# Kernel optimization log

Hardware: AMD Instinct MI355X
Metric: run time of the kernel (lower is better)

Reference implementation:

```python
import jax, jax.numpy as jnp
import numpy as np

BETA = 0.5
LAMBDA = 0.5
EPS = 1e-24


def setup_inputs() -> dict:
    key = jax.random.key(0)
    k1, k2 = jax.random.split(key)
    seq = jax.random.normal(k1, (32, 512, 128), dtype=jnp.float32)
    fism_items = jax.random.normal(k2, (32, 2048, 128), dtype=jnp.float32)
    return {"seq": seq, "fism_items": fism_items}


def reference(seq, fism_items):
    # scores: [B, L, N]
    w = jnp.einsum('bld,bnd->bln', seq, fism_items)
    w_shift = w - jnp.max(w, axis=-1, keepdims=True)
    exp_w = jnp.exp(w_shift)
    exp_sum = jnp.sum(exp_w, axis=-1, keepdims=True)
    if BETA != 1.0:
        exp_sum = jnp.power(exp_sum, jnp.float32(BETA))
    att = exp_w / (exp_sum + EPS)  # power-normalized softmax
    att_vecs = jnp.einsum('bln,bnd->bld', att, fism_items)
    if LAMBDA < 1:
        return seq * (1.0 - LAMBDA) + seq * att_vecs * LAMBDA
    return seq * att_vecs
```

## Files before the change

### kernel.cpp

```cpp
#include <hip/hip_runtime.h>
#include <hip/hip_bf16.h>
#include <math.h>

typedef _Float16 half8  __attribute__((ext_vector_type(8)));
typedef _Float16 half4v __attribute__((ext_vector_type(4)));
typedef __fp16   fp16x2 __attribute__((ext_vector_type(2)));
typedef float    f32x4  __attribute__((ext_vector_type(4)));
typedef float    f32x16 __attribute__((ext_vector_type(16)));
typedef int      i32x2v __attribute__((ext_vector_type(2)));

#define DDIM 128
#define LQ   512
#define NKV  2048
#define KVB  64
#define NIT  8

union U32H2 { unsigned u; fp16x2 h; };
union PW    { unsigned u[4]; half8 h; };

__device__ __forceinline__ float xmax64(float v) {
  i32x2v r = __builtin_amdgcn_permlane32_swap(__float_as_int(v), __float_as_int(v), false, false);
  return fmaxf(__int_as_float(r[0]), __int_as_float(r[1]));
}
__device__ __forceinline__ float xsum64(float v) {
  i32x2v r = __builtin_amdgcn_permlane32_swap(__float_as_int(v), __float_as_int(v), false, false);
  return __int_as_float(r[0]) + __int_as_float(r[1]);
}

__global__ __launch_bounds__(512, 2)
void gattn(const float* __restrict__ seq, const float* __restrict__ fism,
           float* __restrict__ out)
{
  const int tid  = threadIdx.x;
  const int lane = tid & 63;
  const int wv   = tid >> 6;
  const int wq   = wv & 1;
  const int kvq  = wv >> 1;
  const int l31  = lane & 31;
  const int hi   = lane >> 5;

  const int swz = (blockIdx.x & 7) * 32 + (blockIdx.x >> 3);
  const int b   = swz >> 3;
  const int qb  = (swz & 7) * 64;

  const float* seqB = seq  + (size_t)b * LQ * DDIM;
  const float* fisB = fism + (size_t)b * NKV * DDIM;
  float*       outB = out  + (size_t)b * LQ * DDIM;

  __shared__ _Float16 Ksh[4][KVB * DDIM];
  __shared__ _Float16 VTsh[4][(DDIM/2) * 128];
  __shared__ float    stats[4][2][32][3];

  half8 qf[8];
  {
    const int qrow = qb + wq * 32 + l31;
    #pragma unroll
    for (int c = 0; c < 8; ++c) {
      const float* p = seqB + (size_t)qrow * DDIM + c * 16 + hi * 8;
      float4 a  = *(const float4*)p;
      float4 b2 = *(const float4*)(p + 4);
      half8 h;
      h[0]=(_Float16)a.x;  h[1]=(_Float16)a.y;  h[2]=(_Float16)a.z;  h[3]=(_Float16)a.w;
      h[4]=(_Float16)b2.x; h[5]=(_Float16)b2.y; h[6]=(_Float16)b2.z; h[7]=(_Float16)b2.w;
      qf[c] = h;
    }
  }

  const int sp   = tid >> 3;
  const int dgrp = tid & 7;
  const int qstg = sp >> 4;
  const int spc  = sp & 15;

  f32x16 acc[4];
  #pragma unroll
  for (int dt = 0; dt < 4; ++dt)
    #pragma unroll
    for (int i = 0; i < 16; ++i) acc[dt][i] = 0.f;

  float m_run = -INFINITY, tmax = -INFINITY, S_run = 0.f;

  auto write_stage = [&](const float4* v) {
    #pragma unroll
    for (int r = 0; r < 4; ++r) {
      const int row = 4*spc + r;
      #pragma unroll
      for (int hh = 0; hh < 2; ++hh) {
        const float4 x = v[r*4 + hh*2];
        const float4 y = v[r*4 + hh*2 + 1];
        half8 h;
        h[0]=(_Float16)x.x; h[1]=(_Float16)x.y; h[2]=(_Float16)x.z; h[3]=(_Float16)x.w;
        h[4]=(_Float16)y.x; h[5]=(_Float16)y.y; h[6]=(_Float16)y.z; h[7]=(_Float16)y.w;
        const int idx = row*DDIM + ((dgrp*16 + hh*8) ^ (8*(row & 15)));
        *(half8*)&Ksh[qstg][idx] = h;
      }
    }
    #pragma unroll
    for (int k = 0; k < 16; ++k) {
      const int d = dgrp*16 + k;
      const int dRow = d >> 1, dSub = d & 1;
      half4v pk;
      #pragma unroll
      for (int r = 0; r < 4; ++r)
        pk[r] = (_Float16)(((const float*)&v[r*4 + (k>>2)])[k&3]);
      const int idx = dRow*128 + ((dSub*64 + 4*spc) ^ (8*(dRow & 15)));
      *(half4v*)&VTsh[qstg][idx] = pk;
    }
  };

  auto load_glb = [&](float4* v, int t) {
    const float* src = fisB + (size_t)(qstg*(NKV/4) + t*KVB) * DDIM;
    #pragma unroll
    for (int r = 0; r < 4; ++r)
      #pragma unroll
      for (int k = 0; k < 4; ++k)
        v[r*4+k] = *(const float4*)(src + (size_t)(4*spc + r)*DDIM + dgrp*16 + k*4);
  };

  {
    float4 stg[16];
    load_glb(stg, 0);
    write_stage(stg);
  }

  for (int t = 0; t < NIT; ++t) {
    __syncthreads();
    float4 nxt[16];
    const bool have = (t + 1 < NIT);
    if (have) load_glb(nxt, t + 1);

    f32x16 sv[2];
    #pragma unroll
    for (int ns = 0; ns < 2; ++ns) {
      f32x16 x;
      #pragma unroll
      for (int i = 0; i < 16; ++i) x[i] = 0.f;
      const int row = ns*32 + l31;
      const int sw  = 8*(row & 15);
      #pragma unroll
      for (int c = 0; c < 8; ++c) {
        const int idx = row*DDIM + ((c*16 + hi*8) ^ sw);
        half8 kf = *(const half8*)&Ksh[kvq][idx];
        x = __builtin_amdgcn_mfma_f32_32x32x16_f16(kf, qf[c], x, 0, 0, 0);
      }
      sv[ns] = x;
    }

    float mx[16];
    #pragma unroll
    for (int i = 0; i < 16; ++i) mx[i] = fmaxf(sv[0][i], sv[1][i]);
    #pragma unroll
    for (int st = 8; st > 0; st >>= 1)
      #pragma unroll
      for (int i = 0; i < st; ++i) mx[i] = fmaxf(mx[i], mx[i+st]);
    const float cmax = xmax64(mx[0]);
    tmax = fmaxf(tmax, cmax);
    if (__any(cmax > m_run + 8.f)) {
      const float mn = fmaxf(m_run, cmax);
      const float sc = __expf(m_run - mn);
      S_run *= sc;
      m_run = mn;
      #pragma unroll
      for (int dt = 0; dt < 4; ++dt) acc[dt] *= sc;
    }
    float ts[16];
    #pragma unroll
    for (int i = 0; i < 16; ++i) {
      const float p0 = __expf(sv[0][i] - m_run);
      const float p1 = __expf(sv[1][i] - m_run);
      sv[0][i] = p0; sv[1][i] = p1;
      ts[i] = p0 + p1;
    }
    #pragma unroll
    for (int st = 8; st > 0; st >>= 1)
      #pragma unroll
      for (int i = 0; i < st; ++i) ts[i] += ts[i+st];
    S_run += xsum64(ts[0]);

    PW pw[4];
    #pragma unroll
    for (int ns = 0; ns < 2; ++ns)
      #pragma unroll
      for (int b0 = 0; b0 < 2; ++b0) {
        U32H2 t0, t1, t2, t3;
        t0.h = __builtin_amdgcn_cvt_pkrtz(sv[ns][8*b0+0], sv[ns][8*b0+1]);
        t1.h = __builtin_amdgcn_cvt_pkrtz(sv[ns][8*b0+2], sv[ns][8*b0+3]);
        t2.h = __builtin_amdgcn_cvt_pkrtz(sv[ns][8*b0+4], sv[ns][8*b0+5]);
        t3.h = __builtin_amdgcn_cvt_pkrtz(sv[ns][8*b0+6], sv[ns][8*b0+7]);
        i32x2v r0 = __builtin_amdgcn_permlane32_swap((int)t0.u, (int)t2.u, false, false);
        i32x2v r1 = __builtin_amdgcn_permlane32_swap((int)t1.u, (int)t3.u, false, false);
        const int kb = 2*ns + b0;
        pw[kb].u[0] = (unsigned)r0[0];
        pw[kb].u[1] = (unsigned)r1[0];
        pw[kb].u[2] = (unsigned)r0[1];
        pw[kb].u[3] = (unsigned)r1[1];
      }

    #pragma unroll
    for (int dt = 0; dt < 4; ++dt) {
      const int d    = dt*32 + l31;
      const int dRow = d >> 1, dSub = d & 1;
      const int sw   = 8*(dRow & 15);
      #pragma unroll
      for (int kb = 0; kb < 4; ++kb) {
        const int idx = dRow*128 + ((dSub*64 + kb*16 + hi*8) ^ sw);
        half8 vtf = *(const half8*)&VTsh[kvq][idx];
        acc[dt] = __builtin_amdgcn_mfma_f32_32x32x16_f16(vtf, pw[kb].h, acc[dt], 0, 0, 0);
      }
    }

    __syncthreads();
    if (have) write_stage(nxt);
  }

  __syncthreads();

  float* Kf  = (float*)&Ksh[0][0];
  float* VTf = (float*)&VTsh[0][0];
  if (kvq != 0) {
    const int rgn = (kvq - 1) * 2 + wq;
    float* base = (rgn < 4) ? (Kf + rgn * 4096) : (VTf + (rgn - 4) * 4096);
    #pragma unroll
    for (int dt = 0; dt < 4; ++dt)
      #pragma unroll
      for (int rg = 0; rg < 4; ++rg) {
        f32x4 v = {acc[dt][4*rg+0], acc[dt][4*rg+1], acc[dt][4*rg+2], acc[dt][4*rg+3]};
        *(f32x4*)&base[lane*64 + (((dt*4+rg) ^ (lane & 15)) * 4)] = v;
      }
    if (lane < 32) {
      stats[kvq][wq][lane][0] = m_run;
      stats[kvq][wq][lane][1] = S_run;
      stats[kvq][wq][lane][2] = tmax;
    }
  }
  __syncthreads();

  if (kvq == 0) {
    float mj[4], Sj[4], tj[4];
    mj[0] = m_run; Sj[0] = S_run; tj[0] = tmax;
    #pragma unroll
    for (int j = 1; j < 4; ++j) {
      mj[j] = stats[j][wq][l31][0];
      Sj[j] = stats[j][wq][l31][1];
      tj[j] = stats[j][wq][l31][2];
    }
    const float M = fmaxf(fmaxf(tj[0], tj[1]), fmaxf(tj[2], tj[3]));
    float fj[4], den = 0.f;
    #pragma unroll
    for (int j = 0; j < 4; ++j) { fj[j] = __expf(mj[j] - M); den += fj[j] * Sj[j]; }
    const float rs = rsqrtf(den);
    #pragma unroll
    for (int j = 0; j < 4; ++j) fj[j] *= rs;

    const int qrow = qb + wq*32 + l31;
    #pragma unroll
    for (int dt = 0; dt < 4; ++dt) {
      #pragma unroll
      for (int rg = 0; rg < 4; ++rg) {
        f32x4 av = {acc[dt][4*rg+0], acc[dt][4*rg+1], acc[dt][4*rg+2], acc[dt][4*rg+3]};
        av *= fj[0];
        #pragma unroll
        for (int j = 1; j < 4; ++j) {
          const int rgn = (j - 1) * 2 + wq;
          const float* base = (rgn < 4) ? (Kf + rgn * 4096) : (VTf + (rgn - 4) * 4096);
          const f32x4 pj = *(const f32x4*)&base[lane*64 + (((dt*4+rg) ^ (lane & 15)) * 4)];
          av += pj * fj[j];
        }
        const int d0 = dt*32 + rg*8 + hi*4;
        const float4 s = *(const float4*)&seqB[(size_t)qrow * DDIM + d0];
        float4 o;
        o.x = 0.5f * s.x * (1.f + av[0]);
        o.y = 0.5f * s.y * (1.f + av[1]);
        o.z = 0.5f * s.z * (1.f + av[2]);
        o.w = 0.5f * s.w * (1.f + av[3]);
        *(float4*)&outB[(size_t)qrow * DDIM + d0] = o;
      }
    }
  }
}

extern "C" void kernel_launch(void* const* d_in, const int* in_sizes, int n_in,
                              void* d_out, int out_size, void* d_ws, size_t ws_size,
                              hipStream_t stream) {
  const float* seq  = (const float*)d_in[0];
  const float* fism = (const float*)d_in[1];
  float* out = (float*)d_out;
  gattn<<<dim3(256), dim3(512), 0, stream>>>(seq, fism, out);
}
```

Measured before the change: 61.54 us.

## Precompute fp16 K and transposed V in workspace, stream via LDS DMA

```diff
diff --git a/kernel.cpp b/kernel.cpp
--- a/kernel.cpp
+++ b/kernel.cpp
@@ -12,7 +12,7 @@
 #define DDIM 128
 #define LQ   512
 #define NKV  2048
-#define KVB  64
+#define NB   32
 #define NIT  8
 
 union U32H2 { unsigned u; fp16x2 h; };
@@ -27,9 +27,335 @@
   return __int_as_float(r[0]) + __int_as_float(r[1]);
 }
 
+__device__ __forceinline__ void dma16(const void* g, void* l) {
+  __builtin_amdgcn_global_load_lds(
+      (const __attribute__((address_space(1))) unsigned int*)g,
+      (__attribute__((address_space(3))) unsigned int*)l, 16, 0, 0);
+}
+
+__global__ __launch_bounds__(256)
+void prep(const float* __restrict__ fism, _Float16* __restrict__ K16,
+          _Float16* __restrict__ VT16)
+{
+  __shared__ _Float16 T[64 * DDIM];
+  const int tid = threadIdx.x;
+  const int bb  = blockIdx.x >> 5;
+  const int kv0 = (blockIdx.x & 31) * 64;
+  {
+    const int r  = tid >> 2;
+    const int cq = tid & 3;
+    const float* src = fism + ((size_t)(bb*NKV + kv0 + r) * DDIM + cq*32);
+    _Float16*    kd  = K16  + ((size_t)(bb*NKV + kv0 + r) * DDIM + cq*32);
+    float4 v[8];
+    #pragma unroll
+    for (int k = 0; k < 8; ++k) v[k] = ((const float4*)src)[k];
+    _Float16 h[32];
+    #pragma unroll
+    for (int k = 0; k < 8; ++k) {
+      h[4*k+0] = (_Float16)v[k].x; h[4*k+1] = (_Float16)v[k].y;
+      h[4*k+2] = (_Float16)v[k].z; h[4*k+3] = (_Float16)v[k].w;
+    }
+    #pragma unroll
+    for (int k = 0; k < 4; ++k) ((half8*)kd)[k] = *(half8*)&h[8*k];
+    #pragma unroll
+    for (int j = 0; j < 32; ++j) {
+      const int d = cq*32 + j;
+      T[d*64 + (((r>>3) ^ (d&7))<<3) + (r&7)] = h[j];
+    }
+  }
+  __syncthreads();
+  {
+    const int d  = tid >> 1;
+    const int kh = tid & 1;
+    _Float16* vd = VT16 + ((size_t)(bb*DDIM + d) * NKV + kv0 + kh*32);
+    #pragma unroll
+    for (int u = 0; u < 4; ++u) {
+      const int k8 = kh*4 + u;
+      ((half8*)vd)[u] = *(half8*)&T[d*64 + ((k8 ^ (d&7))<<3)];
+    }
+  }
+}
+
+#define QOFF   131072
+#define SAOFF  147456
+#define SBOFF  151552
+
+__global__ __launch_bounds__(1024, 4)
+void gattn(const float* __restrict__ seq, const _Float16* __restrict__ K16,
+           const _Float16* __restrict__ VT16, float* __restrict__ out)
+{
+  __shared__ __align__(16) unsigned char POOL[155648];
+
+  const int tid  = threadIdx.x;
+  const int lane = tid & 63;
+  const int wv   = tid >> 6;
+  const int wq   = wv & 1;
+  const int kvp  = wv >> 1;
+  const int kvq  = kvp >> 1;
+  const int ns   = kvp & 1;
+  const int l31  = lane & 31;
+  const int hi   = lane >> 5;
+
+  const int swz = (blockIdx.x & 7) * 32 + (blockIdx.x >> 3);
+  const int b   = swz >> 3;
+  const int qb  = (swz & 7) * 64;
+
+  const float* seqB = seq + (size_t)b * LQ * DDIM;
+  float*       outB = out + (size_t)b * LQ * DDIM;
+  const _Float16* K16b  = K16  + (size_t)b * NKV * DDIM;
+  const _Float16* VT16b = VT16 + (size_t)b * DDIM * NKV;
+
+  {
+    const int row = tid >> 4, sp = tid & 15;
+    const int s = sp ^ (row & 15);
+    const float* qsrc = seqB + (size_t)(qb + row) * DDIM + s*8;
+    float4 a = ((const float4*)qsrc)[0], b2 = ((const float4*)qsrc)[1];
+    _Float16 hq[8];
+    hq[0]=(_Float16)a.x;  hq[1]=(_Float16)a.y;  hq[2]=(_Float16)a.z;  hq[3]=(_Float16)a.w;
+    hq[4]=(_Float16)b2.x; hq[5]=(_Float16)b2.y; hq[6]=(_Float16)b2.z; hq[7]=(_Float16)b2.w;
+    *(half8*)&POOL[QOFF + tid*16] = *(half8*)hq;
+  }
+
+  int off[8];
+  const bool isK = (wv < 8);
+  const int w8 = wv & 7;
+  if (isK) {
+    #pragma unroll
+    for (int i = 0; i < 8; ++i) {
+      const int unit = w8*512 + i*64 + lane;
+      const int q = unit >> 10, row = (unit >> 4) & 63, sp = unit & 15;
+      const int s = sp ^ (row & 15);
+      off[i] = (q*512 + row)*128 + s*8;
+    }
+  } else {
+    #pragma unroll
+    for (int i = 0; i < 8; ++i) {
+      const int unit = w8*512 + i*64 + lane;
+      const int q = unit >> 10, dRow = (unit >> 4) & 63, sp = unit & 15;
+      const int s = sp ^ (dRow & 15);
+      const int d = dRow*2 + (s >> 3);
+      off[i] = d*2048 + q*512 + (s & 7)*8;
+    }
+  }
+  const _Float16* sbase = isK ? K16b : VT16b;
+  const int tstride = isK ? 8192 : 64;
+  const int ldsbase = (isK ? 0 : 65536) + w8*8192;
+
+  auto stage = [&](int tt) {
+    const _Float16* s0 = sbase + tt * tstride;
+    #pragma unroll
+    for (int i = 0; i < 8; ++i)
+      dma16(s0 + off[i], &POOL[ldsbase + i*1024]);
+  };
+
+  f32x16 acc[4];
+  #pragma unroll
+  for (int dt = 0; dt < 4; ++dt)
+    #pragma unroll
+    for (int i = 0; i < 16; ++i) acc[dt][i] = 0.f;
+
+  float m_run = -INFINITY, tmax = -INFINITY, S_run = 0.f;
+
+  const int krow   = ns*32 + l31;
+  const int kqbase = kvq*16384 + krow*256;
+  const int kswz   = krow & 15;
+  const int qrow   = wq*32 + l31;
+  const int qbase  = QOFF + qrow*256;
+  const int qswz   = qrow & 15;
+
+  stage(0);
+
+  for (int t = 0; t < NIT; ++t) {
+    __syncthreads();
+
+    f32x16 sv;
+    #pragma unroll
+    for (int i = 0; i < 16; ++i) sv[i] = 0.f;
+    #pragma unroll
+    for (int g2 = 0; g2 < 2; ++g2) {
+      half8 ka[4], qa[4];
+      #pragma unroll
+      for (int c2 = 0; c2 < 4; ++c2) {
+        const int u = 2*(g2*4 + c2) + hi;
+        ka[c2] = *(const half8*)&POOL[kqbase + ((u ^ kswz) << 4)];
+        qa[c2] = *(const half8*)&POOL[qbase  + ((u ^ qswz) << 4)];
+      }
+      #pragma unroll
+      for (int c2 = 0; c2 < 4; ++c2)
+        sv = __builtin_amdgcn_mfma_f32_32x32x16_f16(ka[c2], qa[c2], sv, 0, 0, 0);
+    }
+
+    __syncthreads();
+    if (isK && t + 1 < NIT) stage(t + 1);
+
+    float m8[8];
+    #pragma unroll
+    for (int i = 0; i < 8; ++i) m8[i] = fmaxf(sv[i], sv[i+8]);
+    #pragma unroll
+    for (int st = 4; st > 0; st >>= 1)
+      #pragma unroll
+      for (int i = 0; i < st; ++i) m8[i] = fmaxf(m8[i], m8[i+st]);
+    const float cmax = xmax64(m8[0]);
+    tmax = fmaxf(tmax, cmax);
+    if (__any(cmax > m_run + 8.f)) {
+      const float mn = fmaxf(m_run, cmax);
+      const float sc = __expf(m_run - mn);
+      S_run *= sc;
+      m_run = mn;
+      #pragma unroll
+      for (int dt = 0; dt < 4; ++dt) acc[dt] *= sc;
+    }
+    float ts[8];
+    #pragma unroll
+    for (int i = 0; i < 16; ++i) sv[i] = __expf(sv[i] - m_run);
+    #pragma unroll
+    for (int i = 0; i < 8; ++i) ts[i] = sv[i] + sv[i+8];
+    #pragma unroll
+    for (int st = 4; st > 0; st >>= 1)
+      #pragma unroll
+      for (int i = 0; i < st; ++i) ts[i] += ts[i+st];
+    S_run += xsum64(ts[0]);
+
+    PW pw[2];
+    #pragma unroll
+    for (int b0 = 0; b0 < 2; ++b0) {
+      U32H2 t0, t1, t2, t3;
+      t0.h = __builtin_amdgcn_cvt_pkrtz(sv[8*b0+0], sv[8*b0+1]);
+      t1.h = __builtin_amdgcn_cvt_pkrtz(sv[8*b0+2], sv[8*b0+3]);
+      t2.h = __builtin_amdgcn_cvt_pkrtz(sv[8*b0+4], sv[8*b0+5]);
+      t3.h = __builtin_amdgcn_cvt_pkrtz(sv[8*b0+6], sv[8*b0+7]);
+      i32x2v r0 = __builtin_amdgcn_permlane32_swap((int)t0.u, (int)t2.u, false, false);
+      i32x2v r1 = __builtin_amdgcn_permlane32_swap((int)t1.u, (int)t3.u, false, false);
+      pw[b0].u[0] = (unsigned)r0[0];
+      pw[b0].u[1] = (unsigned)r1[0];
+      pw[b0].u[2] = (unsigned)r0[1];
+      pw[b0].u[3] = (unsigned)r1[1];
+    }
+
+    #pragma unroll
+    for (int dt = 0; dt < 4; ++dt) {
+      const int d    = dt*32 + l31;
+      const int dRow = (d >> 1);
+      const int dSub = d & 1;
+      const int vswz = dRow & 15;
+      const int vbase = 65536 + kvq*16384 + dRow*256;
+      #pragma unroll
+      for (int kb = 0; kb < 2; ++kb) {
+        const int s = dSub*8 + ns*4 + kb*2 + hi;
+        half8 vtf = *(const half8*)&POOL[vbase + ((s ^ vswz) << 4)];
+        acc[dt] = __builtin_amdgcn_mfma_f32_32x32x16_f16(vtf, pw[kb].h, acc[dt], 0, 0, 0);
+      }
+    }
+
+    __syncthreads();
+    if (!isK && t + 1 < NIT) stage(t + 1);
+  }
+
+  float* statsA = (float*)&POOL[SAOFF];
+  float* statsB = (float*)&POOL[SBOFF];
+
+  if (ns == 1) {
+    float* base = (float*)&POOL[(kvq*2 + wq) * 16384];
+    #pragma unroll
+    for (int dt = 0; dt < 4; ++dt)
+      #pragma unroll
+      for (int rg = 0; rg < 4; ++rg) {
+        const int j = dt*4 + rg;
+        f32x4 v = {acc[dt][4*rg+0], acc[dt][4*rg+1], acc[dt][4*rg+2], acc[dt][4*rg+3]};
+        *(f32x4*)&base[lane*64 + ((j ^ (lane & 15)) << 2)] = v;
+      }
+    if (lane < 32) {
+      float* st = &statsA[((kvq*2 + wq)*32 + lane) * 4];
+      st[0] = m_run; st[1] = S_run; st[2] = tmax;
+    }
+  }
+  __syncthreads();
+
+  if (ns == 0) {
+    const float* st = &statsA[((kvq*2 + wq)*32 + l31) * 4];
+    const float m1 = st[0], S1 = st[1], t1 = st[2];
+    const float M2 = fmaxf(m_run, m1);
+    const float e0 = __expf(m_run - M2), e1 = __expf(m1 - M2);
+    S_run = S_run * e0 + S1 * e1;
+    tmax  = fmaxf(tmax, t1);
+    m_run = M2;
+    const float* base = (const float*)&POOL[(kvq*2 + wq) * 16384];
+    #pragma unroll
+    for (int dt = 0; dt < 4; ++dt)
+      #pragma unroll
+      for (int rg = 0; rg < 4; ++rg) {
+        const int j = dt*4 + rg;
+        const f32x4 pj = *(const f32x4*)&base[lane*64 + ((j ^ (lane & 15)) << 2)];
+        #pragma unroll
+        for (int i = 0; i < 4; ++i)
+          acc[dt][4*rg+i] = acc[dt][4*rg+i] * e0 + pj[i] * e1;
+      }
+  }
+  __syncthreads();
+
+  if (ns == 0 && kvq != 0) {
+    float* base = (float*)&POOL[((kvq - 1)*2 + wq) * 16384];
+    #pragma unroll
+    for (int dt = 0; dt < 4; ++dt)
+      #pragma unroll
+      for (int rg = 0; rg < 4; ++rg) {
+        const int j = dt*4 + rg;
+        f32x4 v = {acc[dt][4*rg+0], acc[dt][4*rg+1], acc[dt][4*rg+2], acc[dt][4*rg+3]};
+        *(f32x4*)&base[lane*64 + ((j ^ (lane & 15)) << 2)] = v;
+      }
+    if (lane < 32) {
+      float* st = &statsB[((kvq*2 + wq)*32 + lane) * 4];
+      st[0] = m_run; st[1] = S_run; st[2] = tmax;
+    }
+  }
+  __syncthreads();
+
+  if (ns == 0 && kvq == 0) {
+    float mj[4], Sj[4], tj[4];
+    mj[0] = m_run; Sj[0] = S_run; tj[0] = tmax;
+    #pragma unroll
+    for (int j = 1; j < 4; ++j) {
+      const float* st = &statsB[((j*2 + wq)*32 + l31) * 4];
+      mj[j] = st[0]; Sj[j] = st[1]; tj[j] = st[2];
+    }
+    const float M = fmaxf(fmaxf(tj[0], tj[1]), fmaxf(tj[2], tj[3]));
+    float fj[4], den = 0.f;
+    #pragma unroll
+    for (int j = 0; j < 4; ++j) { fj[j] = __expf(mj[j] - M); den += fj[j] * Sj[j]; }
+    const float rs = rsqrtf(den);
+    #pragma unroll
+    for (int j = 0; j < 4; ++j) fj[j] *= rs;
+
+    const int qrw = qb + wq*32 + l31;
+    #pragma unroll
+    for (int dt = 0; dt < 4; ++dt) {
+      #pragma unroll
+      for (int rg = 0; rg < 4; ++rg) {
+        const int jj = dt*4 + rg;
+        f32x4 av = {acc[dt][4*rg+0], acc[dt][4*rg+1], acc[dt][4*rg+2], acc[dt][4*rg+3]};
+        av *= fj[0];
+        #pragma unroll
+        for (int j = 1; j < 4; ++j) {
+          const float* base = (const float*)&POOL[((j - 1)*2 + wq) * 16384];
+          const f32x4 pj = *(const f32x4*)&base[lane*64 + ((jj ^ (lane & 15)) << 2)];
+          av += pj * fj[j];
+        }
+        const int d0 = dt*32 + rg*8 + hi*4;
+        const float4 s = *(const float4*)&seqB[(size_t)qrw * DDIM + d0];
+        float4 o;
+        o.x = 0.5f * s.x * (1.f + av[0]);
+        o.y = 0.5f * s.y * (1.f + av[1]);
+        o.z = 0.5f * s.z * (1.f + av[2]);
+        o.w = 0.5f * s.w * (1.f + av[3]);
+        *(float4*)&outB[(size_t)qrw * DDIM + d0] = o;
+      }
+    }
+  }
+}
+
 __global__ __launch_bounds__(512, 2)
-void gattn(const float* __restrict__ seq, const float* __restrict__ fism,
-           float* __restrict__ out)
+void gattn_fb(const float* __restrict__ seq, const float* __restrict__ fism,
+              float* __restrict__ out)
 {
   const int tid  = threadIdx.x;
   const int lane = tid & 63;
@@ -47,7 +373,7 @@
   const float* fisB = fism + (size_t)b * NKV * DDIM;
   float*       outB = out  + (size_t)b * LQ * DDIM;
 
-  __shared__ _Float16 Ksh[4][KVB * DDIM];
+  __shared__ _Float16 Ksh[4][64 * DDIM];
   __shared__ _Float16 VTsh[4][(DDIM/2) * 128];
   __shared__ float    stats[4][2][32][3];
 
@@ -108,7 +434,7 @@
   };
 
   auto load_glb = [&](float4* v, int t) {
-    const float* src = fisB + (size_t)(qstg*(NKV/4) + t*KVB) * DDIM;
+    const float* src = fisB + (size_t)(qstg*(NKV/4) + t*64) * DDIM;
     #pragma unroll
     for (int r = 0; r < 4; ++r)
       #pragma unroll
@@ -122,19 +448,19 @@
     write_stage(stg);
   }
 
-  for (int t = 0; t < NIT; ++t) {
+  for (int t = 0; t < 8; ++t) {
     __syncthreads();
     float4 nxt[16];
-    const bool have = (t + 1 < NIT);
+    const bool have = (t + 1 < 8);
     if (have) load_glb(nxt, t + 1);
 
     f32x16 sv[2];
     #pragma unroll
-    for (int ns = 0; ns < 2; ++ns) {
+    for (int nss = 0; nss < 2; ++nss) {
       f32x16 x;
       #pragma unroll
       for (int i = 0; i < 16; ++i) x[i] = 0.f;
-      const int row = ns*32 + l31;
+      const int row = nss*32 + l31;
       const int sw  = 8*(row & 15);
       #pragma unroll
       for (int c = 0; c < 8; ++c) {
@@ -142,7 +468,7 @@
         half8 kf = *(const half8*)&Ksh[kvq][idx];
         x = __builtin_amdgcn_mfma_f32_32x32x16_f16(kf, qf[c], x, 0, 0, 0);
       }
-      sv[ns] = x;
+      sv[nss] = x;
     }
 
     float mx[16];
@@ -178,17 +504,17 @@
 
     PW pw[4];
     #pragma unroll
-    for (int ns = 0; ns < 2; ++ns)
+    for (int nss = 0; nss < 2; ++nss)
       #pragma unroll
       for (int b0 = 0; b0 < 2; ++b0) {
         U32H2 t0, t1, t2, t3;
-        t0.h = __builtin_amdgcn_cvt_pkrtz(sv[ns][8*b0+0], sv[ns][8*b0+1]);
-        t1.h = __builtin_amdgcn_cvt_pkrtz(sv[ns][8*b0+2], sv[ns][8*b0+3]);
-        t2.h = __builtin_amdgcn_cvt_pkrtz(sv[ns][8*b0+4], sv[ns][8*b0+5]);
-        t3.h = __builtin_amdgcn_cvt_pkrtz(sv[ns][8*b0+6], sv[ns][8*b0+7]);
+        t0.h = __builtin_amdgcn_cvt_pkrtz(sv[nss][8*b0+0], sv[nss][8*b0+1]);
+        t1.h = __builtin_amdgcn_cvt_pkrtz(sv[nss][8*b0+2], sv[nss][8*b0+3]);
+        t2.h = __builtin_amdgcn_cvt_pkrtz(sv[nss][8*b0+4], sv[nss][8*b0+5]);
+        t3.h = __builtin_amdgcn_cvt_pkrtz(sv[nss][8*b0+6], sv[nss][8*b0+7]);
         i32x2v r0 = __builtin_amdgcn_permlane32_swap((int)t0.u, (int)t2.u, false, false);
         i32x2v r1 = __builtin_amdgcn_permlane32_swap((int)t1.u, (int)t3.u, false, false);
-        const int kb = 2*ns + b0;
+        const int kb = 2*nss + b0;
         pw[kb].u[0] = (unsigned)r0[0];
         pw[kb].u[1] = (unsigned)r1[0];
         pw[kb].u[2] = (unsigned)r0[1];
@@ -284,5 +610,12 @@
   const float* seq  = (const float*)d_in[0];
   const float* fism = (const float*)d_in[1];
   float* out = (float*)d_out;
-  gattn<<<dim3(256), dim3(512), 0, stream>>>(seq, fism, out);
+  if (ws_size >= 33554432ull) {
+    _Float16* K16  = (_Float16*)d_ws;
+    _Float16* VT16 = K16 + (size_t)NB * NKV * DDIM;
+    prep<<<dim3(1024), dim3(256), 0, stream>>>(fism, K16, VT16);
+    gattn<<<dim3(256), dim3(1024), 0, stream>>>(seq, K16, VT16, out);
+  } else {
+    gattn_fb<<<dim3(256), dim3(512), 0, stream>>>(seq, fism, out);
+  }
 }
```

Result: slower. 86.57 us (+40.7%).
